# Optimization experiments

Hardware: AMD Instinct MI355X
Metric: run time of the kernel (lower is better)

Reference implementation:

```python
import jax, jax.numpy as jnp
import numpy as np

N = 50000      # total nodes
E = 800000     # total edges
B = 512        # number of graphs (batch size)
D_IN, H, D_OUT = 5, 96, 192
EPS = 1e-5


def setup_inputs() -> dict:
    key = jax.random.key(0)
    ks = jax.random.split(key, 20)
    s = lambda d: 1.0 / np.sqrt(d)
    inp = {
        "x": jax.random.normal(ks[0], (N, D_IN), jnp.float32),
        "edge_index": jax.random.randint(ks[1], (2, E), 0, N, jnp.int64),
        "batch": jnp.sort(jax.random.randint(ks[2], (N,), 0, B, jnp.int64)),
        "W_in": jax.random.normal(ks[3], (D_IN, H), jnp.float32) * s(D_IN),
        "b_in": jnp.zeros((H,), jnp.float32),
        "W1": jax.random.normal(ks[4], (H, H), jnp.float32) * s(H),
        "b1": jnp.zeros((H,), jnp.float32),
        "g1": jnp.ones((H,), jnp.float32),
        "be1": jnp.zeros((H,), jnp.float32),
        "W2": jax.random.normal(ks[5], (H, H), jnp.float32) * s(H),
        "b2": jnp.zeros((H,), jnp.float32),
        "g2": jnp.ones((H,), jnp.float32),
        "be2": jnp.zeros((H,), jnp.float32),
        "W_out": jax.random.normal(ks[6], (H, D_OUT), jnp.float32) * s(H),
        "b_out": jnp.zeros((D_OUT,), jnp.float32),
        "ln_g": jnp.ones((D_OUT,), jnp.float32),
        "ln_b": jnp.zeros((D_OUT,), jnp.float32),
    }
    return inp


def gcn_conv(h, W, b, src, dst):
    # PyG GCNConv: h' = D^{-1/2} (A + I) D^{-1/2} (h W) + b, deg from self-looped graph
    h = h @ W                                           # [N, H]
    deg = jnp.ones((N,), h.dtype).at[dst].add(jnp.ones((E,), h.dtype))
    dinv = jax.lax.rsqrt(deg)                           # [N]
    coef = dinv[src] * dinv[dst]                        # [E]
    agg = jnp.zeros_like(h).at[dst].add(h[src] * coef[:, None])
    agg = agg + h * (dinv * dinv)[:, None]              # self-loop term
    return agg + b


def batch_norm(x, g, b):
    m = x.mean(0)
    v = x.var(0)
    return g * (x - m) * jax.lax.rsqrt(v + EPS) + b


def reference(x, edge_index, batch, W_in, b_in, W1, b1, g1, be1, W2, b2, g2, be2,
              W_out, b_out, ln_g, ln_b):
    src, dst = edge_index[0], edge_index[1]
    h = jax.nn.relu(x @ W_in + b_in)
    for (W, bb, g, be) in ((W1, b1, g1, be1), (W2, b2, g2, be2)):
        r = h
        h = gcn_conv(h, W, bb, src, dst)
        h = jax.nn.relu(batch_norm(h, g, be))           # dropout = identity (eval)
        h = h + r
    counts = jnp.zeros((B,), h.dtype).at[batch].add(1.0)
    pooled = jax.ops.segment_sum(h, batch, num_segments=B)
    pooled = pooled / jnp.maximum(counts, 1.0)[:, None]  # global_mean_pool [B, H]
    out = pooled @ W_out + b_out                         # [B, D_OUT]
    mu = out.mean(-1, keepdims=True)
    var = out.var(-1, keepdims=True)
    return ln_g * (out - mu) * jax.lax.rsqrt(var + EPS) + ln_b
```

## Files before the change

### kernel.cpp

```cpp
#include <hip/hip_runtime.h>
#include <hip/hip_bf16.h>
#include <stdint.h>

#define NN 50000
#define EE 800000
#define BB 512
#define HH 96
#define DIN 5
#define DOUT 192
#define EPSV 1e-5f
#define NBANK 32
#define HWS 64
#define NB_GATHER 3125
#define NBUK 512
#define BUKN 98
#define FILLB 128
#define FCHUNK (EE / FILLB)

__device__ inline float blo(uint32_t w) { return __uint_as_float(w << 16); }
__device__ inline float bhi(uint32_t w) { return __uint_as_float(w & 0xffff0000u); }
__device__ inline uint32_t packbf(float a, float b) {
    uint32_t ua = __float_as_uint(a); ua += 0x7fffu + ((ua >> 16) & 1u);
    uint32_t ub = __float_as_uint(b); ub += 0x7fffu + ((ub >> 16) & 1u);
    return (ua >> 16) | (ub & 0xffff0000u);
}

__global__ __launch_bounds__(256) void k_bhist(const int* __restrict__ dst,
                                               int* __restrict__ bkcnt) {
    __shared__ int hist[NBUK];
    int tid = threadIdx.x;
    for (int j = tid; j < NBUK; j += 256) hist[j] = 0;
    __syncthreads();
    int e0 = blockIdx.x * FCHUNK;
    for (int e = e0 + tid; e < e0 + FCHUNK; e += 256) atomicAdd(&hist[dst[e] / BUKN], 1);
    __syncthreads();
    for (int j = tid; j < NBUK; j += 256) if (hist[j]) atomicAdd(&bkcnt[j], hist[j]);
}

__global__ __launch_bounds__(256) void k_bscan(const int* __restrict__ bkcnt,
                                               int* __restrict__ bkbase,
                                               int* __restrict__ bkcur,
                                               float* __restrict__ stats,
                                               int* __restrict__ row_ptr) {
    __shared__ int sc[NBUK + 1];
    int t = threadIdx.x;
    for (int i = t; i < 2 * NBANK * 192; i += 256) stats[i] = 0.0f;
    for (int j = t; j < NBUK; j += 256) sc[j] = bkcnt[j];
    __syncthreads();
    if (t == 0) {
        int c = 0;
        for (int j = 0; j < NBUK; ++j) { int s = sc[j]; sc[j] = c; c += s; }
        sc[NBUK] = c;
        row_ptr[NN] = c;
    }
    __syncthreads();
    for (int j = t; j <= NBUK; j += 256) bkbase[j] = sc[j];
    for (int j = t; j < NBUK; j += 256) bkcur[j] = sc[j];
}

__global__ __launch_bounds__(256) void k_bscat(const int* __restrict__ src,
                                               const int* __restrict__ dst,
                                               int* __restrict__ bkcur,
                                               uint32_t* __restrict__ ebuf) {
    __shared__ int hist[NBUK], bbase[NBUK], cnt[NBUK];
    int tid = threadIdx.x;
    int e0 = blockIdx.x * FCHUNK, e1 = e0 + FCHUNK;
    for (int j = tid; j < NBUK; j += 256) { hist[j] = 0; cnt[j] = 0; }
    __syncthreads();
    for (int e = e0 + tid; e < e1; e += 256) atomicAdd(&hist[dst[e] / BUKN], 1);
    __syncthreads();
    for (int j = tid; j < NBUK; j += 256) bbase[j] = hist[j] ? atomicAdd(&bkcur[j], hist[j]) : 0;
    __syncthreads();
    for (int e = e0 + tid; e < e1; e += 256) {
        int d = dst[e];
        int b = d / BUKN;
        int off = atomicAdd(&cnt[b], 1);
        ebuf[bbase[b] + off] = (uint32_t)src[e] | ((uint32_t)(d - b * BUKN) << 16);
    }
}

__global__ __launch_bounds__(256) void k_csr(const uint32_t* __restrict__ ebuf,
                                             const int* __restrict__ bkbase,
                                             int* __restrict__ row_ptr,
                                             int* __restrict__ col,
                                             float* __restrict__ dinv) {
    __shared__ int cnt[BUKN], base[BUKN], lcur[BUKN];
    int b = blockIdx.x, tid = threadIdx.x;
    int node0 = b * BUKN;
    if (node0 >= NN) return;
    int nn = min(BUKN, NN - node0);
    int ebase = bkbase[b], eend = bkbase[b + 1];
    for (int j = tid; j < nn; j += 256) { cnt[j] = 0; lcur[j] = 0; }
    __syncthreads();
    for (int i = ebase + tid; i < eend; i += 256) atomicAdd(&cnt[ebuf[i] >> 16], 1);
    __syncthreads();
    if (tid == 0) {
        int c = 0;
        for (int j = 0; j < nn; ++j) { base[j] = c; c += cnt[j]; }
    }
    __syncthreads();
    for (int j = tid; j < nn; j += 256) {
        row_ptr[node0 + j] = ebase + base[j];
        dinv[node0 + j] = rsqrtf((float)cnt[j] + 1.0f);
    }
    for (int i = ebase + tid; i < eend; i += 256) {
        uint32_t w = ebuf[i];
        int dr = (int)(w >> 16);
        int off = atomicAdd(&lcur[dr], 1);
        col[ebase + base[dr] + off] = (int)(w & 0xffffu);
    }
}

__global__ __launch_bounds__(256) void k_gemm_in(const float* __restrict__ x,
                                                 const float* __restrict__ Win,
                                                 const float* __restrict__ bin,
                                                 const float* __restrict__ W1,
                                                 const float* __restrict__ dinv,
                                                 float* __restrict__ h0,
                                                 uint32_t* __restrict__ hwb) {
    __shared__ float sAT[96][68];
    __shared__ float sW[96 * 96];
    int tid = threadIdx.x;
    int row0 = blockIdx.x * 64;

    for (int i = tid; i < 96 * 96; i += 256) sW[i] = W1[i];

    {
        int r = tid >> 2, q = tid & 3;
        int j0q = q * 24;
        int gr = row0 + r;
        float xv[5];
#pragma unroll
        for (int k = 0; k < DIN; ++k) xv[k] = (gr < NN) ? x[gr * DIN + k] : 0.0f;
        float hv[24];
#pragma unroll
        for (int jj = 0; jj < 24; ++jj) {
            float acc = bin[j0q + jj];
#pragma unroll
            for (int k = 0; k < DIN; ++k) acc += xv[k] * Win[k * 96 + j0q + jj];
            hv[jj] = fmaxf(acc, 0.0f);
            sAT[j0q + jj][r] = hv[jj];
        }
        if (gr < NN) {
#pragma unroll
            for (int jj = 0; jj < 24; jj += 4)
                *reinterpret_cast<float4*>(&h0[(size_t)gr * 96 + j0q + jj]) =
                    make_float4(hv[jj], hv[jj + 1], hv[jj + 2], hv[jj + 3]);
        }
    }
    __syncthreads();

    int tc = tid & 15, tr = tid >> 4;
    int r0 = tr * 4, j0 = tc * 6;
    float acc[4][6];
#pragma unroll
    for (int i = 0; i < 4; ++i)
#pragma unroll
        for (int j = 0; j < 6; ++j) acc[i][j] = 0.0f;

    for (int k = 0; k < 96; ++k) {
        float4 a = *reinterpret_cast<const float4*>(&sAT[k][r0]);
        const float* wr = &sW[k * 96 + j0];
        float b0 = wr[0], b1 = wr[1], b2 = wr[2], b3 = wr[3], b4 = wr[4], b5 = wr[5];
        float av[4] = {a.x, a.y, a.z, a.w};
#pragma unroll
        for (int i = 0; i < 4; ++i) {
            acc[i][0] += av[i] * b0; acc[i][1] += av[i] * b1; acc[i][2] += av[i] * b2;
            acc[i][3] += av[i] * b3; acc[i][4] += av[i] * b4; acc[i][5] += av[i] * b5;
        }
    }
#pragma unroll
    for (int i = 0; i < 4; ++i) {
        int gr = row0 + r0 + i;
        if (gr < NN) {
            float dv = dinv[gr];
            uint32_t* wp = &hwb[(size_t)gr * HWS + tc * 3];
            wp[0] = packbf(acc[i][0] * dv, acc[i][1] * dv);
            wp[1] = packbf(acc[i][2] * dv, acc[i][3] * dv);
            wp[2] = packbf(acc[i][4] * dv, acc[i][5] * dv);
        }
    }
}

__global__ __launch_bounds__(256) void k_gather(const uint32_t* __restrict__ hwb,
                                                const float* __restrict__ dinv,
                                                const int* __restrict__ row_ptr,
                                                const int* __restrict__ col,
                                                float* __restrict__ agg,
                                                float* __restrict__ stats) {
    int tid = threadIdx.x;
    int t = tid & 15, slot = tid >> 4;
    int n = blockIdx.x * 16 + slot;

    const uint32_t* rn = hwb + (size_t)n * HWS;
    uint2 w01 = *reinterpret_cast<const uint2*>(rn + 2 * t);
    uint32_t w2 = rn[32 + t];
    float a0 = blo(w01.x), a1 = bhi(w01.x);
    float a2 = blo(w01.y), a3 = bhi(w01.y);
    float a4 = blo(w2),    a5 = bhi(w2);

    int beg = row_ptr[n], end = row_ptr[n + 1];
    int p = beg;
    for (; p + 3 < end; p += 4) {
        int s0 = col[p], s1 = col[p + 1], s2 = col[p + 2], s3 = col[p + 3];
        const uint32_t* r0 = hwb + (size_t)s0 * HWS;
        const uint32_t* r1 = hwb + (size_t)s1 * HWS;
        const uint32_t* r2 = hwb + (size_t)s2 * HWS;
        const uint32_t* r3 = hwb + (size_t)s3 * HWS;
        uint2 u0 = *reinterpret_cast<const uint2*>(r0 + 2 * t); uint32_t v0 = r0[32 + t];
        uint2 u1 = *reinterpret_cast<const uint2*>(r1 + 2 * t); uint32_t v1 = r1[32 + t];
        uint2 u2 = *reinterpret_cast<const uint2*>(r2 + 2 * t); uint32_t v2 = r2[32 + t];
        uint2 u3 = *reinterpret_cast<const uint2*>(r3 + 2 * t); uint32_t v3 = r3[32 + t];
        a0 += blo(u0.x); a1 += bhi(u0.x); a2 += blo(u0.y); a3 += bhi(u0.y);
        a4 += blo(v0);   a5 += bhi(v0);
        a0 += blo(u1.x); a1 += bhi(u1.x); a2 += blo(u1.y); a3 += bhi(u1.y);
        a4 += blo(v1);   a5 += bhi(v1);
        a0 += blo(u2.x); a1 += bhi(u2.x); a2 += blo(u2.y); a3 += bhi(u2.y);
        a4 += blo(v2);   a5 += bhi(v2);
        a0 += blo(u3.x); a1 += bhi(u3.x); a2 += blo(u3.y); a3 += bhi(u3.y);
        a4 += blo(v3);   a5 += bhi(v3);
    }
    for (; p < end; ++p) {
        const uint32_t* rs = hwb + (size_t)col[p] * HWS;
        uint2 u = *reinterpret_cast<const uint2*>(rs + 2 * t);
        uint32_t v = rs[32 + t];
        a0 += blo(u.x); a1 += bhi(u.x);
        a2 += blo(u.y); a3 += bhi(u.y);
        a4 += blo(v);   a5 += bhi(v);
    }
    float dn = dinv[n];
    a0 *= dn; a1 *= dn; a2 *= dn; a3 *= dn; a4 *= dn; a5 *= dn;

    float* an = agg + (size_t)n * 96;
    *reinterpret_cast<float4*>(&an[4 * t])      = make_float4(a0, a1, a2, a3);
    *reinterpret_cast<float2*>(&an[64 + 2 * t]) = make_float2(a4, a5);

    __shared__ float red[2][96];
    if (tid < 96) { red[0][tid] = 0.0f; red[1][tid] = 0.0f; }
    __syncthreads();
    int colsv[6] = {4 * t, 4 * t + 1, 4 * t + 2, 4 * t + 3, 64 + 2 * t, 64 + 2 * t + 1};
    float cs[6] = {a0, a1, a2, a3, a4, a5};
#pragma unroll
    for (int k = 0; k < 6; ++k) {
        atomicAdd(&red[0][colsv[k]], cs[k]);
        atomicAdd(&red[1][colsv[k]], cs[k] * cs[k]);
    }
    __syncthreads();
    float* bank = stats + (blockIdx.x & (NBANK - 1)) * 192;
    if (tid < 96) {
        atomicAdd(&bank[tid], red[0][tid]);
        atomicAdd(&bank[96 + tid], red[1][tid]);
    }
}

__global__ __launch_bounds__(256) void k_gemm_bn(const float* __restrict__ agg,
                                                 const float* __restrict__ hprev,
                                                 const float* __restrict__ stats,
                                                 const float* __restrict__ g,
                                                 const float* __restrict__ be,
                                                 const float* __restrict__ W,
                                                 const float* __restrict__ dinv,
                                                 float* __restrict__ hnew,
                                                 uint32_t* __restrict__ hwb) {
    __shared__ float sAT[96][68];
    __shared__ float sW[96 * 96];
    __shared__ float ssc[96], ssh[96];
    int tid = threadIdx.x;
    int row0 = blockIdx.x * 64;

    for (int i = tid; i < 96 * 96; i += 256) sW[i] = W[i];
    if (tid < 96) {
        float s = 0.0f, s2 = 0.0f;
#pragma unroll
        for (int k = 0; k < NBANK; ++k) { s += stats[k * 192 + tid]; s2 += stats[k * 192 + 96 + tid]; }
        float m = s * (1.0f / NN);
        float var = s2 * (1.0f / NN) - m * m;
        float sc = g[tid] * rsqrtf(var + EPSV);
        ssc[tid] = sc;
        ssh[tid] = be[tid] - m * sc;
    }
    __syncthreads();

    for (int i = tid; i < 64 * 24; i += 256) {
        int r = i / 24, qq = i % 24;
        int gr = row0 + r, c = qq * 4;
        float4 v = make_float4(0.0f, 0.0f, 0.0f, 0.0f);
        if (gr < NN) {
            float4 a = *reinterpret_cast<const float4*>(&agg[(size_t)gr * 96 + c]);
            float4 pv = *reinterpret_cast<const float4*>(&hprev[(size_t)gr * 96 + c]);
            v.x = fmaxf(a.x * ssc[c]     + ssh[c],     0.0f) + pv.x;
            v.y = fmaxf(a.y * ssc[c + 1] + ssh[c + 1], 0.0f) + pv.y;
            v.z = fmaxf(a.z * ssc[c + 2] + ssh[c + 2], 0.0f) + pv.z;
            v.w = fmaxf(a.w * ssc[c + 3] + ssh[c + 3], 0.0f) + pv.w;
            *reinterpret_cast<float4*>(&hnew[(size_t)gr * 96 + c]) = v;
        }
        sAT[c][r] = v.x; sAT[c + 1][r] = v.y; sAT[c + 2][r] = v.z; sAT[c + 3][r] = v.w;
    }
    __syncthreads();

    int tc = tid & 15, tr = tid >> 4;
    int r0 = tr * 4, j0 = tc * 6;
    float acc[4][6];
#pragma unroll
    for (int i = 0; i < 4; ++i)
#pragma unroll
        for (int j = 0; j < 6; ++j) acc[i][j] = 0.0f;

    for (int k = 0; k < 96; ++k) {
        float4 a = *reinterpret_cast<const float4*>(&sAT[k][r0]);
        const float* wr = &sW[k * 96 + j0];
        float b0 = wr[0], b1 = wr[1], b2 = wr[2], b3 = wr[3], b4 = wr[4], b5 = wr[5];
        float av[4] = {a.x, a.y, a.z, a.w};
#pragma unroll
        for (int i = 0; i < 4; ++i) {
            acc[i][0] += av[i] * b0; acc[i][1] += av[i] * b1; acc[i][2] += av[i] * b2;
            acc[i][3] += av[i] * b3; acc[i][4] += av[i] * b4; acc[i][5] += av[i] * b5;
        }
    }
#pragma unroll
    for (int i = 0; i < 4; ++i) {
        int gr = row0 + r0 + i;
        if (gr < NN) {
            float dv = dinv[gr];
            uint32_t* wp = &hwb[(size_t)gr * HWS + tc * 3];
            wp[0] = packbf(acc[i][0] * dv, acc[i][1] * dv);
            wp[1] = packbf(acc[i][2] * dv, acc[i][3] * dv);
            wp[2] = packbf(acc[i][4] * dv, acc[i][5] * dv);
        }
    }
}

__device__ inline int lower_bound_i(const int* __restrict__ a, int n, int v) {
    int lo = 0, hi = n;
    while (lo < hi) { int mid = (lo + hi) >> 1; if (a[mid] < v) lo = mid + 1; else hi = mid; }
    return lo;
}

__global__ __launch_bounds__(384) void k_out(const float* __restrict__ agg,
                                             const float* __restrict__ hprev,
                                             const float* __restrict__ stats,
                                             const float* __restrict__ g,
                                             const float* __restrict__ be,
                                             const int* __restrict__ batch,
                                             const float* __restrict__ Wout,
                                             const float* __restrict__ bout,
                                             const float* __restrict__ lg,
                                             const float* __restrict__ lb,
                                             float* __restrict__ out) {
    __shared__ float ssc[96], ssh[96];
    __shared__ float sp4[4][96];
    __shared__ float sp[96];
    __shared__ float svals[192];
    __shared__ float smv[2];
    int b = blockIdx.x, t = threadIdx.x;
    if (t < 96) {
        float s = 0.0f, s2 = 0.0f;
#pragma unroll
        for (int k = 0; k < NBANK; ++k) { s += stats[k * 192 + t]; s2 += stats[k * 192 + 96 + t]; }
        float m = s * (1.0f / NN);
        float var = s2 * (1.0f / NN) - m * m;
        float sc = g[t] * rsqrtf(var + EPSV);
        ssc[t] = sc;
        ssh[t] = be[t] - m * sc;
    }
    int lo = lower_bound_i(batch, NN, b);
    int hi = lower_bound_i(batch, NN, b + 1);
    __syncthreads();

    int colc = t % 96, qr = t / 96;
    float scc = ssc[colc], shc = ssh[colc];
    float accp = 0.0f;
    for (int r = lo + qr; r < hi; r += 4) {
        size_t idx = (size_t)r * 96 + colc;
        accp += fmaxf(agg[idx] * scc + shc, 0.0f) + hprev[idx];
    }
    sp4[qr][colc] = accp;
    __syncthreads();
    if (t < 96) {
        float inv = (hi > lo) ? 1.0f / (float)(hi - lo) : 0.0f;
        sp[t] = (sp4[0][t] + sp4[1][t] + sp4[2][t] + sp4[3][t]) * inv;
    }
    __syncthreads();

    float acc = 0.0f;
    if (t < 192) {
        acc = bout[t];
        for (int k = 0; k < 96; ++k) acc += sp[k] * Wout[k * 192 + t];
        svals[t] = acc;
    }
    __syncthreads();
    if (t < 64) {
        float a0 = svals[t], a1 = svals[t + 64], a2 = svals[t + 128];
        float s = a0 + a1 + a2;
        float s2 = a0 * a0 + a1 * a1 + a2 * a2;
        for (int o = 32; o > 0; o >>= 1) {
            s += __shfl_down(s, o, 64);
            s2 += __shfl_down(s2, o, 64);
        }
        if (t == 0) { smv[0] = s * (1.0f / 192.0f); smv[1] = s2 * (1.0f / 192.0f); }
    }
    __syncthreads();
    if (t < 192) {
        float m = smv[0];
        float var = smv[1] - m * m;
        float rr = rsqrtf(var + EPSV);
        out[b * 192 + t] = lg[t] * (acc - m) * rr + lb[t];
    }
}

extern "C" void kernel_launch(void* const* d_in, const int* in_sizes, int n_in,
                              void* d_out, int out_size, void* d_ws, size_t ws_size,
                              hipStream_t stream) {
    const float* x    = (const float*)d_in[0];
    const int*   ei   = (const int*)  d_in[1];
    const int*   batch= (const int*)  d_in[2];
    const float* Win  = (const float*)d_in[3];
    const float* bin  = (const float*)d_in[4];
    const float* W1   = (const float*)d_in[5];
    const float* g1   = (const float*)d_in[7];
    const float* be1  = (const float*)d_in[8];
    const float* W2   = (const float*)d_in[9];
    const float* g2   = (const float*)d_in[11];
    const float* be2  = (const float*)d_in[12];
    const float* Wout = (const float*)d_in[13];
    const float* bout = (const float*)d_in[14];
    const float* lg   = (const float*)d_in[15];
    const float* lb   = (const float*)d_in[16];
    const int* src = ei;
    const int* dst = ei + EE;

    float*    ws_f   = (float*)d_ws;
    float*    h0     = ws_f;
    float*    h1     = h0 + (size_t)NN * HH;
    float*    agg    = h1 + (size_t)NN * HH;
    float*    dinv   = agg + (size_t)NN * HH;
    float*    stats  = dinv + NN;
    uint32_t* hwb    = (uint32_t*)(stats + 2 * NBANK * 192);
    int*      row_ptr= (int*)(hwb + (size_t)NN * HWS);
    int*      bkcnt  = row_ptr + NN + 1;
    int*      bkbase = bkcnt + NBUK;
    int*      bkcur  = bkbase + NBUK + 1;
    int*      col    = bkcur + NBUK;
    uint32_t* ebuf   = (uint32_t*)agg;

    const int TB = 256;
    float* stats1 = stats;
    float* stats2 = stats + NBANK * 192;

    hipMemsetAsync(bkcnt, 0, NBUK * sizeof(int), stream);
    k_bhist<<<FILLB, TB, 0, stream>>>(dst, bkcnt);
    k_bscan<<<1, TB, 0, stream>>>(bkcnt, bkbase, bkcur, stats, row_ptr);
    k_bscat<<<FILLB, TB, 0, stream>>>(src, dst, bkcur, ebuf);
    k_csr<<<NBUK, TB, 0, stream>>>(ebuf, bkbase, row_ptr, col, dinv);

    k_gemm_in<<<(NN + 63) / 64, TB, 0, stream>>>(x, Win, bin, W1, dinv, h0, hwb);
    k_gather<<<NB_GATHER, TB, 0, stream>>>(hwb, dinv, row_ptr, col, agg, stats1);

    k_gemm_bn<<<(NN + 63) / 64, TB, 0, stream>>>(agg, h0, stats1, g1, be1, W2, dinv, h1, hwb);
    k_gather<<<NB_GATHER, TB, 0, stream>>>(hwb, dinv, row_ptr, col, agg, stats2);

    k_out<<<BB, 384, 0, stream>>>(agg, h1, stats2, g2, be2, batch, Wout, bout, lg, lb,
                                  (float*)d_out);
}
```

Measured before the change: 268.7 us.

## Store intermediates in bf16 and degree-sort nodes for gather load balance

Switches the h0, h1 and agg intermediates from fp32 to packed bf16 rows and shrinks the row stride from 64 to 48 words, which cuts the bytes moved by the gemm, gather and output-pooling kernels. It also adds a three-kernel counting sort of nodes by in-degree, so each gather block handles nodes of similar degree and wavefronts diverge less. The costs are extra small kernel launches and bf16 rounding of the residual and aggregate values, which lowers accuracy.

```diff
diff --git a/kernel.cpp b/kernel.cpp
--- a/kernel.cpp
+++ b/kernel.cpp
@@ -10,8 +10,9 @@
 #define DOUT 192
 #define EPSV 1e-5f
 #define NBANK 32
-#define HWS 64
+#define HWS 48
 #define NB_GATHER 3125
+#define NBLK_SCAN ((NN + 1023) / 1024)
 #define NBUK 512
 #define BUKN 98
 #define FILLB 128
@@ -83,6 +84,7 @@
                                              const int* __restrict__ bkbase,
                                              int* __restrict__ row_ptr,
                                              int* __restrict__ col,
+                                             int* __restrict__ degi,
                                              float* __restrict__ dinv) {
     __shared__ int cnt[BUKN], base[BUKN], lcur[BUKN];
     int b = blockIdx.x, tid = threadIdx.x;
@@ -101,6 +103,7 @@
     __syncthreads();
     for (int j = tid; j < nn; j += 256) {
         row_ptr[node0 + j] = ebase + base[j];
+        degi[node0 + j] = cnt[j];
         dinv[node0 + j] = rsqrtf((float)cnt[j] + 1.0f);
     }
     for (int i = ebase + tid; i < eend; i += 256) {
@@ -111,12 +114,69 @@
     }
 }
 
+__global__ __launch_bounds__(1024) void k_dhist(const int* __restrict__ degi,
+                                                int* __restrict__ histg) {
+    __shared__ int dh[64];
+    int tid = threadIdx.x;
+    if (tid < 64) dh[tid] = 0;
+    __syncthreads();
+    int i = blockIdx.x * 1024 + tid;
+    if (i < NN) atomicAdd(&dh[min(degi[i], 63)], 1);
+    __syncthreads();
+    if (tid < 64) histg[blockIdx.x * 64 + tid] = dh[tid];
+}
+
+__global__ __launch_bounds__(64) void k_dscan(int* __restrict__ histg) {
+    __shared__ int tot[64], binbase[64];
+    int t = threadIdx.x;
+    int s = 0;
+    for (int k = 0; k < NBLK_SCAN; ++k) s += histg[k * 64 + t];
+    tot[t] = s;
+    __syncthreads();
+    if (t == 0) {
+        int c = 0;
+        for (int b2 = 0; b2 < 64; ++b2) { binbase[b2] = c; c += tot[b2]; }
+    }
+    __syncthreads();
+    int c = binbase[t];
+    for (int k = 0; k < NBLK_SCAN; ++k) {
+        int tmp = histg[k * 64 + t];
+        histg[k * 64 + t] = c;
+        c += tmp;
+    }
+}
+
+__global__ __launch_bounds__(1024) void k_dperm(const int* __restrict__ degi,
+                                                const int* __restrict__ histg,
+                                                int* __restrict__ perm) {
+    __shared__ int lcur[64];
+    int tid = threadIdx.x;
+    if (tid < 64) lcur[tid] = histg[blockIdx.x * 64 + tid];
+    __syncthreads();
+    int i = blockIdx.x * 1024 + tid;
+    if (i < NN) {
+        int pos = atomicAdd(&lcur[min(degi[i], 63)], 1);
+        perm[pos] = i;
+    }
+}
+
+__device__ inline void pack24(uint32_t* __restrict__ dstrow, int q,
+                              const float* v, float scale) {
+    uint32_t wv[12];
+#pragma unroll
+    for (int p = 0; p < 12; ++p) wv[p] = packbf(v[2 * p] * scale, v[2 * p + 1] * scale);
+    uint4* dstp = reinterpret_cast<uint4*>(dstrow + q * 12);
+    dstp[0] = make_uint4(wv[0], wv[1], wv[2], wv[3]);
+    dstp[1] = make_uint4(wv[4], wv[5], wv[6], wv[7]);
+    dstp[2] = make_uint4(wv[8], wv[9], wv[10], wv[11]);
+}
+
 __global__ __launch_bounds__(256) void k_gemm_in(const float* __restrict__ x,
                                                  const float* __restrict__ Win,
                                                  const float* __restrict__ bin,
                                                  const float* __restrict__ W1,
                                                  const float* __restrict__ dinv,
-                                                 float* __restrict__ h0,
+                                                 uint32_t* __restrict__ h0b,
                                                  uint32_t* __restrict__ hwb) {
     __shared__ float sAT[96][68];
     __shared__ float sW[96 * 96];
@@ -141,12 +201,7 @@
             hv[jj] = fmaxf(acc, 0.0f);
             sAT[j0q + jj][r] = hv[jj];
         }
-        if (gr < NN) {
-#pragma unroll
-            for (int jj = 0; jj < 24; jj += 4)
-                *reinterpret_cast<float4*>(&h0[(size_t)gr * 96 + j0q + jj]) =
-                    make_float4(hv[jj], hv[jj + 1], hv[jj + 2], hv[jj + 3]);
-        }
+        if (gr < NN) pack24(&h0b[(size_t)gr * HWS], q, hv, 1.0f);
     }
     __syncthreads();
 
@@ -186,11 +241,12 @@
                                                 const float* __restrict__ dinv,
                                                 const int* __restrict__ row_ptr,
                                                 const int* __restrict__ col,
-                                                float* __restrict__ agg,
+                                                const int* __restrict__ perm,
+                                                uint32_t* __restrict__ aggb,
                                                 float* __restrict__ stats) {
     int tid = threadIdx.x;
     int t = tid & 15, slot = tid >> 4;
-    int n = blockIdx.x * 16 + slot;
+    int n = perm[blockIdx.x * 16 + slot];
 
     const uint32_t* rn = hwb + (size_t)n * HWS;
     uint2 w01 = *reinterpret_cast<const uint2*>(rn + 2 * t);
@@ -231,9 +287,9 @@
     float dn = dinv[n];
     a0 *= dn; a1 *= dn; a2 *= dn; a3 *= dn; a4 *= dn; a5 *= dn;
 
-    float* an = agg + (size_t)n * 96;
-    *reinterpret_cast<float4*>(&an[4 * t])      = make_float4(a0, a1, a2, a3);
-    *reinterpret_cast<float2*>(&an[64 + 2 * t]) = make_float2(a4, a5);
+    uint32_t* an = aggb + (size_t)n * HWS;
+    *reinterpret_cast<uint2*>(an + 2 * t) = make_uint2(packbf(a0, a1), packbf(a2, a3));
+    an[32 + t] = packbf(a4, a5);
 
     __shared__ float red[2][96];
     if (tid < 96) { red[0][tid] = 0.0f; red[1][tid] = 0.0f; }
@@ -253,14 +309,14 @@
     }
 }
 
-__global__ __launch_bounds__(256) void k_gemm_bn(const float* __restrict__ agg,
-                                                 const float* __restrict__ hprev,
+__global__ __launch_bounds__(256) void k_gemm_bn(const uint32_t* __restrict__ aggb,
+                                                 const uint32_t* __restrict__ hprevb,
                                                  const float* __restrict__ stats,
                                                  const float* __restrict__ g,
                                                  const float* __restrict__ be,
                                                  const float* __restrict__ W,
                                                  const float* __restrict__ dinv,
-                                                 float* __restrict__ hnew,
+                                                 uint32_t* __restrict__ hnewb,
                                                  uint32_t* __restrict__ hwb) {
     __shared__ float sAT[96][68];
     __shared__ float sW[96 * 96];
@@ -283,18 +339,19 @@
 
     for (int i = tid; i < 64 * 24; i += 256) {
         int r = i / 24, qq = i % 24;
-        int gr = row0 + r, c = qq * 4;
-        float4 v = make_float4(0.0f, 0.0f, 0.0f, 0.0f);
+        int gr = row0 + r, c = qq * 4, w0 = qq * 2;
+        float v0 = 0.0f, v1 = 0.0f, v2 = 0.0f, v3 = 0.0f;
         if (gr < NN) {
-            float4 a = *reinterpret_cast<const float4*>(&agg[(size_t)gr * 96 + c]);
-            float4 pv = *reinterpret_cast<const float4*>(&hprev[(size_t)gr * 96 + c]);
-            v.x = fmaxf(a.x * ssc[c]     + ssh[c],     0.0f) + pv.x;
-            v.y = fmaxf(a.y * ssc[c + 1] + ssh[c + 1], 0.0f) + pv.y;
-            v.z = fmaxf(a.z * ssc[c + 2] + ssh[c + 2], 0.0f) + pv.z;
-            v.w = fmaxf(a.w * ssc[c + 3] + ssh[c + 3], 0.0f) + pv.w;
-            *reinterpret_cast<float4*>(&hnew[(size_t)gr * 96 + c]) = v;
-        }
-        sAT[c][r] = v.x; sAT[c + 1][r] = v.y; sAT[c + 2][r] = v.z; sAT[c + 3][r] = v.w;
+            uint2 aw = *reinterpret_cast<const uint2*>(&aggb[(size_t)gr * HWS + w0]);
+            uint2 pw = *reinterpret_cast<const uint2*>(&hprevb[(size_t)gr * HWS + w0]);
+            v0 = fmaxf(blo(aw.x) * ssc[c]     + ssh[c],     0.0f) + blo(pw.x);
+            v1 = fmaxf(bhi(aw.x) * ssc[c + 1] + ssh[c + 1], 0.0f) + bhi(pw.x);
+            v2 = fmaxf(blo(aw.y) * ssc[c + 2] + ssh[c + 2], 0.0f) + blo(pw.y);
+            v3 = fmaxf(bhi(aw.y) * ssc[c + 3] + ssh[c + 3], 0.0f) + bhi(pw.y);
+            *reinterpret_cast<uint2*>(&hnewb[(size_t)gr * HWS + w0]) =
+                make_uint2(packbf(v0, v1), packbf(v2, v3));
+        }
+        sAT[c][r] = v0; sAT[c + 1][r] = v1; sAT[c + 2][r] = v2; sAT[c + 3][r] = v3;
     }
     __syncthreads();
 
@@ -336,8 +393,8 @@
     return lo;
 }
 
-__global__ __launch_bounds__(384) void k_out(const float* __restrict__ agg,
-                                             const float* __restrict__ hprev,
+__global__ __launch_bounds__(384) void k_out(const uint32_t* __restrict__ aggb,
+                                             const uint32_t* __restrict__ hprevb,
                                              const float* __restrict__ stats,
                                              const float* __restrict__ g,
                                              const float* __restrict__ be,
@@ -348,7 +405,7 @@
                                              const float* __restrict__ lb,
                                              float* __restrict__ out) {
     __shared__ float ssc[96], ssh[96];
-    __shared__ float sp4[4][96];
+    __shared__ float sp8[8][96];
     __shared__ float sp[96];
     __shared__ float svals[192];
     __shared__ float smv[2];
@@ -367,18 +424,25 @@
     int hi = lower_bound_i(batch, NN, b + 1);
     __syncthreads();
 
-    int colc = t % 96, qr = t / 96;
-    float scc = ssc[colc], shc = ssh[colc];
-    float accp = 0.0f;
-    for (int r = lo + qr; r < hi; r += 4) {
-        size_t idx = (size_t)r * 96 + colc;
-        accp += fmaxf(agg[idx] * scc + shc, 0.0f) + hprev[idx];
-    }
-    sp4[qr][colc] = accp;
+    int w = t % 48, qr = t / 48;
+    int c0 = 2 * w, c1 = 2 * w + 1;
+    float sc0 = ssc[c0], sh0 = ssh[c0], sc1 = ssc[c1], sh1 = ssh[c1];
+    float accp0 = 0.0f, accp1 = 0.0f;
+    for (int r = lo + qr; r < hi; r += 8) {
+        uint32_t a = aggb[(size_t)r * HWS + w];
+        uint32_t h = hprevb[(size_t)r * HWS + w];
+        accp0 += fmaxf(blo(a) * sc0 + sh0, 0.0f) + blo(h);
+        accp1 += fmaxf(bhi(a) * sc1 + sh1, 0.0f) + bhi(h);
+    }
+    sp8[qr][c0] = accp0;
+    sp8[qr][c1] = accp1;
     __syncthreads();
     if (t < 96) {
         float inv = (hi > lo) ? 1.0f / (float)(hi - lo) : 0.0f;
-        sp[t] = (sp4[0][t] + sp4[1][t] + sp4[2][t] + sp4[3][t]) * inv;
+        float s = 0.0f;
+#pragma unroll
+        for (int k = 0; k < 8; ++k) s += sp8[k][t];
+        sp[t] = s * inv;
     }
     __syncthreads();
 
@@ -429,19 +493,22 @@
     const int* src = ei;
     const int* dst = ei + EE;
 
-    float*    ws_f   = (float*)d_ws;
-    float*    h0     = ws_f;
-    float*    h1     = h0 + (size_t)NN * HH;
-    float*    agg    = h1 + (size_t)NN * HH;
-    float*    dinv   = agg + (size_t)NN * HH;
+    uint32_t* wsp    = (uint32_t*)d_ws;
+    uint32_t* h0b    = wsp;
+    uint32_t* h1b    = h0b + (size_t)NN * HWS;
+    uint32_t* aggb   = h1b + (size_t)NN * HWS;
+    uint32_t* hwb    = aggb + (size_t)NN * HWS;
+    float*    dinv   = (float*)(hwb + (size_t)NN * HWS);
     float*    stats  = dinv + NN;
-    uint32_t* hwb    = (uint32_t*)(stats + 2 * NBANK * 192);
-    int*      row_ptr= (int*)(hwb + (size_t)NN * HWS);
-    int*      bkcnt  = row_ptr + NN + 1;
+    int*      degi   = (int*)(stats + 2 * NBANK * 192);
+    int*      histg  = degi + NN;
+    int*      row_ptr= histg + NBLK_SCAN * 64;
+    int*      perm   = row_ptr + NN + 1;
+    int*      bkcnt  = perm + NN;
     int*      bkbase = bkcnt + NBUK;
     int*      bkcur  = bkbase + NBUK + 1;
     int*      col    = bkcur + NBUK;
-    uint32_t* ebuf   = (uint32_t*)agg;
+    uint32_t* ebuf   = aggb;
 
     const int TB = 256;
     float* stats1 = stats;
@@ -451,14 +518,17 @@
     k_bhist<<<FILLB, TB, 0, stream>>>(dst, bkcnt);
     k_bscan<<<1, TB, 0, stream>>>(bkcnt, bkbase, bkcur, stats, row_ptr);
     k_bscat<<<FILLB, TB, 0, stream>>>(src, dst, bkcur, ebuf);
-    k_csr<<<NBUK, TB, 0, stream>>>(ebuf, bkbase, row_ptr, col, dinv);
-
-    k_gemm_in<<<(NN + 63) / 64, TB, 0, stream>>>(x, Win, bin, W1, dinv, h0, hwb);
-    k_gather<<<NB_GATHER, TB, 0, stream>>>(hwb, dinv, row_ptr, col, agg, stats1);
-
-    k_gemm_bn<<<(NN + 63) / 64, TB, 0, stream>>>(agg, h0, stats1, g1, be1, W2, dinv, h1, hwb);
-    k_gather<<<NB_GATHER, TB, 0, stream>>>(hwb, dinv, row_ptr, col, agg, stats2);
-
-    k_out<<<BB, 384, 0, stream>>>(agg, h1, stats2, g2, be2, batch, Wout, bout, lg, lb,
+    k_csr<<<NBUK, TB, 0, stream>>>(ebuf, bkbase, row_ptr, col, degi, dinv);
+    k_dhist<<<NBLK_SCAN, 1024, 0, stream>>>(degi, histg);
+    k_dscan<<<1, 64, 0, stream>>>(histg);
+    k_dperm<<<NBLK_SCAN, 1024, 0, stream>>>(degi, histg, perm);
+
+    k_gemm_in<<<(NN + 63) / 64, TB, 0, stream>>>(x, Win, bin, W1, dinv, h0b, hwb);
+    k_gather<<<NB_GATHER, TB, 0, stream>>>(hwb, dinv, row_ptr, col, perm, aggb, stats1);
+
+    k_gemm_bn<<<(NN + 63) / 64, TB, 0, stream>>>(aggb, h0b, stats1, g1, be1, W2, dinv, h1b, hwb);
+    k_gather<<<NB_GATHER, TB, 0, stream>>>(hwb, dinv, row_ptr, col, perm, aggb, stats2);
+
+    k_out<<<BB, 384, 0, stream>>>(aggb, h1b, stats2, g2, be2, batch, Wout, bout, lg, lb,
                                   (float*)d_out);
 }
```

New measurement: 258.0 us. -4.0%, faster.
